# Performance work log

Measured on AMD Instinct MI355X. Metric: run time of the kernel, lower is better.

The kernel has to match this reference:

```python
import jax, jax.numpy as jnp
import numpy as np

N = 50000          # nodes
E = 800000         # edges (avg in-degree 16)
IN_FEATS = 256
H = 4              # num_heads
D = 32             # out_feats per head
NEG_SLOPE = 0.2


def setup_inputs() -> dict:
    key = jax.random.key(0)
    k1, k2, k3, k4, k5, k6 = jax.random.split(key, 6)
    feat = jax.random.normal(k1, (N, IN_FEATS), dtype=jnp.float32)
    src = jax.random.randint(k2, (E,), 0, N, dtype=jnp.int32)
    dst = jax.random.randint(k3, (E,), 0, N, dtype=jnp.int32)
    # parameters (xavier-ish scale)
    W = jax.random.normal(k4, (IN_FEATS, H * D), dtype=jnp.float32) * (2.0 / (IN_FEATS + H * D)) ** 0.5
    attn_l = jax.random.normal(k5, (H, D), dtype=jnp.float32) * 0.1
    attn_r = jax.random.normal(k6, (H, D), dtype=jnp.float32) * 0.1
    bias = jnp.zeros((H * D,), dtype=jnp.float32)
    return {"feat": feat, "src": src, "dst": dst, "W": W,
            "attn_l": attn_l, "attn_r": attn_r, "bias": bias}


def reference(feat, src, dst, W, attn_l, attn_r, bias):
    # dense projection: [N, H, D]
    ft = (feat @ W).reshape(N, H, D)
    # per-node attention logits: [N, H]
    el = jnp.einsum('nhd,hd->nh', ft, attn_l)
    er = jnp.einsum('nhd,hd->nh', ft, attn_r)
    # SDDMM u_add_v + leaky relu: per-edge scores [E, H]
    e = jax.nn.leaky_relu(el[src] + er[dst], negative_slope=NEG_SLOPE)
    # edge softmax over incoming edges of each dst node (segment softmax)
    m = jax.ops.segment_max(e, dst, num_segments=N)          # [N, H], -inf for empty
    e_exp = jnp.exp(e - m[dst])                               # [E, H]
    s = jax.ops.segment_sum(e_exp, dst, num_segments=N)       # [N, H]
    a = e_exp / s[dst]                                        # [E, H]
    # SpMM u_mul_e: weighted aggregation to dst nodes
    rst = jax.ops.segment_sum(ft[src] * a[:, :, None], dst, num_segments=N)  # [N, H, D]
    rst = rst + bias.reshape(1, H, D)
    return rst
```

## Files before the change

kernel.cpp:

```cpp
#include <hip/hip_runtime.h>
#include <hip/hip_bf16.h>
#include <math.h>

#define N_NODES 50000
#define N_EDGES 800000
#define IN_F 256
#define HD 128
#define NHEAD 4
#define NB_SCAN 196

typedef __attribute__((ext_vector_type(8))) short bf16x8;
typedef __attribute__((ext_vector_type(4))) float f32x4;

__device__ __forceinline__ float lrelu(float x){ return x > 0.f ? x : 0.2f * x; }

__device__ __forceinline__ unsigned short f32_to_bf16_rn(float x){
    union { float f; unsigned int u; } v; v.f = x;
    unsigned int r = v.u + 0x7FFFu + ((v.u >> 16) & 1u);
    return (unsigned short)(r >> 16);
}
__device__ __forceinline__ float bf16_to_f32(unsigned short h){
    union { unsigned int u; float f; } v; v.u = ((unsigned int)h) << 16;
    return v.f;
}
__device__ __forceinline__ float bflo(unsigned int u){
    union { unsigned int x; float f; } v; v.x = u << 16; return v.f;
}
__device__ __forceinline__ float bfhi(unsigned int u){
    union { unsigned int x; float f; } v; v.x = u & 0xFFFF0000u; return v.f;
}

__global__ void zero_ints(int* __restrict__ p, int n){
    int i = blockIdx.x * blockDim.x + threadIdx.x;
    if (i < n) p[i] = 0;
}

__global__ __launch_bounds__(256) void wsplit_kernel(const float* __restrict__ W,
                                                     unsigned short* __restrict__ Wt_hi,
                                                     unsigned short* __restrict__ Wt_lo){
    int gid = blockIdx.x * 256 + threadIdx.x;
    int n = gid >> 8;
    int k = gid & 255;
    float x = W[(size_t)k * HD + n];
    unsigned short h = f32_to_bf16_rn(x);
    float r = x - bf16_to_f32(h);
    unsigned short l = f32_to_bf16_rn(r);
    Wt_hi[gid] = h;
    Wt_lo[gid] = l;
}

__global__ __launch_bounds__(256) void gemm_kernel(const float* __restrict__ feat,
                                                   const unsigned short* __restrict__ Wt_hi,
                                                   const unsigned short* __restrict__ Wt_lo,
                                                   const float* __restrict__ attn_l,
                                                   const float* __restrict__ attn_r,
                                                   unsigned short* __restrict__ ftb,
                                                   float* __restrict__ el,
                                                   float* __restrict__ er){
    __shared__ unsigned short Ah[128][72];
    __shared__ unsigned short Al[128][72];
    __shared__ unsigned short Bh[128][72];
    __shared__ unsigned short Bl[128][72];

    const int tid  = threadIdx.x;
    const int lane = tid & 63;
    const int wave = tid >> 6;
    const int wrow = wave * 32;
    const int lrow = lane & 15;
    const int lkh  = (lane >> 4) * 8;
    const int row0 = blockIdx.x * 128;

    f32x4 acc[2][8];
#pragma unroll
    for (int i = 0; i < 2; i++)
#pragma unroll
        for (int j = 0; j < 8; j++) acc[i][j] = (f32x4){0.f, 0.f, 0.f, 0.f};

    const int srow = tid >> 1;
    const int skh  = (tid & 1) * 32;

    for (int kc = 0; kc < 4; ++kc){
        const int k0 = kc * 64;
        {
            int gr = row0 + srow;
            const float* fp = feat + (size_t)gr * IN_F + k0 + skh;
            unsigned short* ah = &Ah[srow][skh];
            unsigned short* al = &Al[srow][skh];
#pragma unroll
            for (int u = 0; u < 8; ++u){
                float4 v = make_float4(0.f,0.f,0.f,0.f);
                if (gr < N_NODES) v = *(const float4*)(fp + 4 * u);
                ushort4 h, l;
                h.x = f32_to_bf16_rn(v.x); l.x = f32_to_bf16_rn(v.x - bf16_to_f32(h.x));
                h.y = f32_to_bf16_rn(v.y); l.y = f32_to_bf16_rn(v.y - bf16_to_f32(h.y));
                h.z = f32_to_bf16_rn(v.z); l.z = f32_to_bf16_rn(v.z - bf16_to_f32(h.z));
                h.w = f32_to_bf16_rn(v.w); l.w = f32_to_bf16_rn(v.w - bf16_to_f32(h.w));
                *(ushort4*)(ah + 4 * u) = h;
                *(ushort4*)(al + 4 * u) = l;
            }
        }
        {
            const unsigned short* bh = Wt_hi + srow * 256 + k0 + skh;
            const unsigned short* bl = Wt_lo + srow * 256 + k0 + skh;
#pragma unroll
            for (int u = 0; u < 4; ++u){
                *(uint4*)(&Bh[srow][skh + 8 * u]) = *(const uint4*)(bh + 8 * u);
                *(uint4*)(&Bl[srow][skh + 8 * u]) = *(const uint4*)(bl + 8 * u);
            }
        }
        __syncthreads();
#pragma unroll
        for (int kk = 0; kk < 2; ++kk){
            const int kb = kk * 32 + lkh;
            bf16x8 ah0 = *(const bf16x8*)(&Ah[wrow + lrow][kb]);
            bf16x8 ah1 = *(const bf16x8*)(&Ah[wrow + 16 + lrow][kb]);
            bf16x8 al0 = *(const bf16x8*)(&Al[wrow + lrow][kb]);
            bf16x8 al1 = *(const bf16x8*)(&Al[wrow + 16 + lrow][kb]);
#pragma unroll
            for (int nf = 0; nf < 8; ++nf){
                bf16x8 bh = *(const bf16x8*)(&Bh[nf * 16 + lrow][kb]);
                bf16x8 bl = *(const bf16x8*)(&Bl[nf * 16 + lrow][kb]);
                acc[0][nf] = __builtin_amdgcn_mfma_f32_16x16x32_bf16(ah0, bh, acc[0][nf], 0, 0, 0);
                acc[1][nf] = __builtin_amdgcn_mfma_f32_16x16x32_bf16(ah1, bh, acc[1][nf], 0, 0, 0);
                acc[0][nf] = __builtin_amdgcn_mfma_f32_16x16x32_bf16(ah0, bl, acc[0][nf], 0, 0, 0);
                acc[1][nf] = __builtin_amdgcn_mfma_f32_16x16x32_bf16(ah1, bl, acc[1][nf], 0, 0, 0);
                acc[0][nf] = __builtin_amdgcn_mfma_f32_16x16x32_bf16(al0, bh, acc[0][nf], 0, 0, 0);
                acc[1][nf] = __builtin_amdgcn_mfma_f32_16x16x32_bf16(al1, bh, acc[1][nf], 0, 0, 0);
            }
        }
        __syncthreads();
    }
    float alv[8], arv[8];
#pragma unroll
    for (int nf = 0; nf < 8; ++nf){
        alv[nf] = attn_l[lrow + nf * 16];
        arv[nf] = attn_r[lrow + nf * 16];
    }
#pragma unroll
    for (int mf = 0; mf < 2; ++mf){
#pragma unroll
        for (int r = 0; r < 4; ++r){
            int gr = row0 + wrow + mf * 16 + (lane >> 4) * 4 + r;
            if (gr < N_NODES){
                unsigned short* op = ftb + (size_t)gr * HD + lrow;
#pragma unroll
                for (int nf = 0; nf < 8; ++nf) op[nf * 16] = f32_to_bf16_rn(acc[mf][nf][r]);
            }
            float pl0 = acc[mf][0][r] * alv[0] + acc[mf][1][r] * alv[1];
            float pl1 = acc[mf][2][r] * alv[2] + acc[mf][3][r] * alv[3];
            float pl2 = acc[mf][4][r] * alv[4] + acc[mf][5][r] * alv[5];
            float pl3 = acc[mf][6][r] * alv[6] + acc[mf][7][r] * alv[7];
            float pr0 = acc[mf][0][r] * arv[0] + acc[mf][1][r] * arv[1];
            float pr1 = acc[mf][2][r] * arv[2] + acc[mf][3][r] * arv[3];
            float pr2 = acc[mf][4][r] * arv[4] + acc[mf][5][r] * arv[5];
            float pr3 = acc[mf][6][r] * arv[6] + acc[mf][7][r] * arv[7];
#pragma unroll
            for (int m = 1; m <= 8; m <<= 1){
                pl0 += __shfl_xor(pl0, m, 64); pl1 += __shfl_xor(pl1, m, 64);
                pl2 += __shfl_xor(pl2, m, 64); pl3 += __shfl_xor(pl3, m, 64);
                pr0 += __shfl_xor(pr0, m, 64); pr1 += __shfl_xor(pr1, m, 64);
                pr2 += __shfl_xor(pr2, m, 64); pr3 += __shfl_xor(pr3, m, 64);
            }
            if ((lane & 15) == 0 && gr < N_NODES){
                *(float4*)(el + (size_t)gr * NHEAD) = make_float4(pl0, pl1, pl2, pl3);
                *(float4*)(er + (size_t)gr * NHEAD) = make_float4(pr0, pr1, pr2, pr3);
            }
        }
    }
}

__global__ void degree_kernel(const int* __restrict__ dst, int* __restrict__ deg,
                              int* __restrict__ rank){
    int e = blockIdx.x * blockDim.x + threadIdx.x;
    if (e < N_EDGES) rank[e] = atomicAdd(&deg[dst[e]], 1);
}

__global__ __launch_bounds__(256) void scan_part(const int* __restrict__ deg,
                                                 int* __restrict__ row_off,
                                                 int* __restrict__ blk_sums){
    __shared__ int lds[256];
    int tid = threadIdx.x;
    int i = blockIdx.x * 256 + tid;
    int v = (i < N_NODES) ? deg[i] : 0;
    int x = v;
    lds[tid] = x;
    __syncthreads();
    for (int off = 1; off < 256; off <<= 1){
        int t = (tid >= off) ? lds[tid - off] : 0;
        __syncthreads();
        x += t;
        lds[tid] = x;
        __syncthreads();
    }
    if (i < N_NODES) row_off[i] = x - v;
    if (tid == 255) blk_sums[blockIdx.x] = x;
}

__global__ __launch_bounds__(256) void scan_mid(int* __restrict__ blk_sums,
                                                int* __restrict__ blk_off){
    __shared__ int lds[256];
    int tid = threadIdx.x;
    int v = (tid < NB_SCAN) ? blk_sums[tid] : 0;
    int x = v;
    lds[tid] = x;
    __syncthreads();
    for (int off = 1; off < 256; off <<= 1){
        int t = (tid >= off) ? lds[tid - off] : 0;
        __syncthreads();
        x += t;
        lds[tid] = x;
        __syncthreads();
    }
    blk_off[tid] = x - v;
}

__global__ __launch_bounds__(256) void scan_add(int* __restrict__ row_off,
                                                const int* __restrict__ blk_off){
    int i = blockIdx.x * 256 + threadIdx.x;
    if (i < N_NODES) row_off[i] += blk_off[blockIdx.x];
    if (blockIdx.x == 0 && threadIdx.x == 0) row_off[N_NODES] = N_EDGES;
}

__global__ void scatter_kernel(const int* __restrict__ src, const int* __restrict__ dst,
                               const int* __restrict__ rank, const int* __restrict__ row_off,
                               int* __restrict__ csr_src){
    int e = blockIdx.x * blockDim.x + threadIdx.x;
    if (e >= N_EDGES) return;
    csr_src[row_off[dst[e]] + rank[e]] = src[e];
}

__global__ __launch_bounds__(256) void aggregate_kernel(const unsigned short* __restrict__ ftb,
                                                        const int* __restrict__ csr_src,
                                                        const float* __restrict__ el,
                                                        const float* __restrict__ er,
                                                        const int* __restrict__ row_off,
                                                        const float* __restrict__ bias,
                                                        float* __restrict__ out){
    __shared__ float lw[4][64][4];
    __shared__ int   ls[4][64];

    const int wv   = threadIdx.x >> 6;
    const int n    = blockIdx.x * 4 + wv;
    const int lane = threadIdx.x & 63;
    const int g    = lane >> 4;
    const int l    = lane & 15;
    const int h    = l >> 2;
    const int beg  = row_off[n], end = row_off[n + 1];
    const float4 ern = *(const float4*)(er + (size_t)n * NHEAD);

    float a[8];
#pragma unroll
    for (int k = 0; k < 8; ++k) a[k] = 0.f;
    float wsum = 0.f;

    for (int base = beg; base < end; base += 64){
        int cnt = end - base; if (cnt > 64) cnt = 64;
        float4 w4 = make_float4(0.f, 0.f, 0.f, 0.f);
        int s_l = 0;
        if (lane < cnt){
            s_l = csr_src[base + lane];
            float4 elv = *(const float4*)(el + (size_t)s_l * NHEAD);
            w4.x = __expf(lrelu(elv.x + ern.x));
            w4.y = __expf(lrelu(elv.y + ern.y));
            w4.z = __expf(lrelu(elv.z + ern.z));
            w4.w = __expf(lrelu(elv.w + ern.w));
        }
        ls[wv][lane] = s_l;
        *(float4*)(&lw[wv][lane][0]) = w4;
        asm volatile("s_waitcnt lgkmcnt(0)" ::: "memory");
        __builtin_amdgcn_sched_barrier(0);
        for (int j0 = 0; j0 < cnt; j0 += 4){
            int j = j0 + g;
            float w = lw[wv][j][h];
            int   s = ls[wv][j];
            uint4 f = *(const uint4*)(ftb + (size_t)s * HD + 8 * l);
            a[0] += w * bflo(f.x); a[1] += w * bfhi(f.x);
            a[2] += w * bflo(f.y); a[3] += w * bfhi(f.y);
            a[4] += w * bflo(f.z); a[5] += w * bfhi(f.z);
            a[6] += w * bflo(f.w); a[7] += w * bfhi(f.w);
            wsum += w;
        }
        __builtin_amdgcn_sched_barrier(0);
    }
#pragma unroll
    for (int m = 16; m <= 32; m <<= 1){
#pragma unroll
        for (int k = 0; k < 8; ++k) a[k] += __shfl_xor(a[k], m, 64);
        wsum += __shfl_xor(wsum, m, 64);
    }
    float inv = (end > beg) ? 1.f / wsum : 0.f;
    if (g < 2){
        int col = 8 * l + 4 * g;
        float4 b4 = *(const float4*)(bias + col);
        float4 o;
        o.x = a[4 * g + 0] * inv + b4.x;
        o.y = a[4 * g + 1] * inv + b4.y;
        o.z = a[4 * g + 2] * inv + b4.z;
        o.w = a[4 * g + 3] * inv + b4.w;
        *(float4*)(out + (size_t)n * HD + col) = o;
    }
}

extern "C" void kernel_launch(void* const* d_in, const int* in_sizes, int n_in,
                              void* d_out, int out_size, void* d_ws, size_t ws_size,
                              hipStream_t stream){
    const float* feat   = (const float*)d_in[0];
    const int*   src    = (const int*)  d_in[1];
    const int*   dst    = (const int*)  d_in[2];
    const float* W      = (const float*)d_in[3];
    const float* attn_l = (const float*)d_in[4];
    const float* attn_r = (const float*)d_in[5];
    const float* bias   = (const float*)d_in[6];
    float* out = (float*)d_out;
    char*  ws  = (char*)d_ws;

    unsigned short* ftb = (unsigned short*)(ws + 0);
    float* el      = (float*)(ws + 12800000);
    float* er      = (float*)(ws + 13600000);
    int*   deg     = (int*)  (ws + 14400000);
    int*   rank    = (int*)  (ws + 14600000);
    int*   row_off = (int*)  (ws + 17800000);
    int*   csr_src = (int*)  (ws + 18000064);

    unsigned short* Wt_hi = (unsigned short*)csr_src;
    unsigned short* Wt_lo = Wt_hi + 32768;
    int* blk_sums = (int*)(((char*)csr_src) + 131072);
    int* blk_off  = blk_sums + 256;

    zero_ints<<<(N_NODES + 255) / 256, 256, 0, stream>>>(deg, N_NODES);
    wsplit_kernel<<<128, 256, 0, stream>>>(W, Wt_hi, Wt_lo);
    gemm_kernel<<<(N_NODES + 127) / 128, 256, 0, stream>>>(feat, Wt_hi, Wt_lo,
                                                           attn_l, attn_r, ftb, el, er);
    degree_kernel<<<(N_EDGES + 255) / 256, 256, 0, stream>>>(dst, deg, rank);
    scan_part<<<NB_SCAN, 256, 0, stream>>>(deg, row_off, blk_sums);
    scan_mid<<<1, 256, 0, stream>>>(blk_sums, blk_off);
    scan_add<<<NB_SCAN, 256, 0, stream>>>(row_off, blk_off);
    scatter_kernel<<<(N_EDGES + 255) / 256, 256, 0, stream>>>(src, dst, rank, row_off, csr_src);
    aggregate_kernel<<<(N_NODES + 3) / 4, 256, 0, stream>>>(ftb, csr_src, el, er,
                                                            row_off, bias, out);
}
```

Baseline: 225.2 us.

## Load GEMM A fragments directly to registers and shrink row tile to 64

The projection GEMM now has each lane load its own fp32 feat fragment straight from global memory into registers and split it into bf16 hi/lo there, so the A tile no longer goes through LDS. B is stored in LDS pre-swizzled in MFMA fragment order. The row tile per block drops from 128 to 64, giving each wave one 16-row MFMA tile instead of two, and launch bounds ask for 4 blocks per CU. The aim is less LDS traffic and pressure, more occupancy and more blocks; the cost is that each block reloads W into LDS for half as many rows.

```diff
diff --git a/kernel.cpp b/kernel.cpp
--- a/kernel.cpp
+++ b/kernel.cpp
@@ -8,6 +8,7 @@
 #define HD 128
 #define NHEAD 4
 #define NB_SCAN 196
+#define GBM 64
 
 typedef __attribute__((ext_vector_type(8))) short bf16x8;
 typedef __attribute__((ext_vector_type(4))) float f32x4;
@@ -49,83 +50,67 @@
     Wt_lo[gid] = l;
 }
 
-__global__ __launch_bounds__(256) void gemm_kernel(const float* __restrict__ feat,
-                                                   const unsigned short* __restrict__ Wt_hi,
-                                                   const unsigned short* __restrict__ Wt_lo,
-                                                   const float* __restrict__ attn_l,
-                                                   const float* __restrict__ attn_r,
-                                                   unsigned short* __restrict__ ftb,
-                                                   float* __restrict__ el,
-                                                   float* __restrict__ er){
-    __shared__ unsigned short Ah[128][72];
-    __shared__ unsigned short Al[128][72];
-    __shared__ unsigned short Bh[128][72];
-    __shared__ unsigned short Bl[128][72];
+__global__ __launch_bounds__(256, 4) void gemm_kernel(const float* __restrict__ feat,
+                                                      const unsigned short* __restrict__ Wt_hi,
+                                                      const unsigned short* __restrict__ Wt_lo,
+                                                      const float* __restrict__ attn_l,
+                                                      const float* __restrict__ attn_r,
+                                                      unsigned short* __restrict__ ftb,
+                                                      float* __restrict__ el,
+                                                      float* __restrict__ er){
+    __shared__ unsigned short Bh[2][8][64][8];
+    __shared__ unsigned short Bl[2][8][64][8];
 
     const int tid  = threadIdx.x;
     const int lane = tid & 63;
-    const int wave = tid >> 6;
-    const int wrow = wave * 32;
-    const int lrow = lane & 15;
-    const int lkh  = (lane >> 4) * 8;
-    const int row0 = blockIdx.x * 128;
-
-    f32x4 acc[2][8];
-#pragma unroll
-    for (int i = 0; i < 2; i++)
-#pragma unroll
-        for (int j = 0; j < 8; j++) acc[i][j] = (f32x4){0.f, 0.f, 0.f, 0.f};
-
-    const int srow = tid >> 1;
-    const int skh  = (tid & 1) * 32;
+    const int wv   = tid >> 6;
+    const int r    = lane & 15;
+    const int g    = lane >> 4;
+    const int arow = blockIdx.x * GBM + wv * 16 + r;
+    const bool rowok = (arow < N_NODES);
+    const float* arp = feat + (size_t)arow * IN_F + g * 8;
+
+    f32x4 acc[8];
+#pragma unroll
+    for (int j = 0; j < 8; ++j) acc[j] = (f32x4){0.f, 0.f, 0.f, 0.f};
 
     for (int kc = 0; kc < 4; ++kc){
         const int k0 = kc * 64;
-        {
-            int gr = row0 + srow;
-            const float* fp = feat + (size_t)gr * IN_F + k0 + skh;
-            unsigned short* ah = &Ah[srow][skh];
-            unsigned short* al = &Al[srow][skh];
-#pragma unroll
-            for (int u = 0; u < 8; ++u){
-                float4 v = make_float4(0.f,0.f,0.f,0.f);
-                if (gr < N_NODES) v = *(const float4*)(fp + 4 * u);
-                ushort4 h, l;
-                h.x = f32_to_bf16_rn(v.x); l.x = f32_to_bf16_rn(v.x - bf16_to_f32(h.x));
-                h.y = f32_to_bf16_rn(v.y); l.y = f32_to_bf16_rn(v.y - bf16_to_f32(h.y));
-                h.z = f32_to_bf16_rn(v.z); l.z = f32_to_bf16_rn(v.z - bf16_to_f32(h.z));
-                h.w = f32_to_bf16_rn(v.w); l.w = f32_to_bf16_rn(v.w - bf16_to_f32(h.w));
-                *(ushort4*)(ah + 4 * u) = h;
-                *(ushort4*)(al + 4 * u) = l;
+#pragma unroll
+        for (int i = 0; i < 4; ++i){
+            int u  = tid * 4 + i;
+            int l2 = u & 63;
+            int fn = (u >> 6) & 7;
+            int kb = u >> 9;
+            int nn = fn * 16 + (l2 & 15);
+            int kk = k0 + kb * 32 + (l2 >> 4) * 8;
+            *(uint4*)(&Bh[kb][fn][l2][0]) = *(const uint4*)(Wt_hi + nn * 256 + kk);
+            *(uint4*)(&Bl[kb][fn][l2][0]) = *(const uint4*)(Wt_lo + nn * 256 + kk);
+        }
+        __syncthreads();
+#pragma unroll
+        for (int kb = 0; kb < 2; ++kb){
+            float4 v0 = make_float4(0.f, 0.f, 0.f, 0.f), v1 = v0;
+            if (rowok){
+                const float* fp = arp + k0 + kb * 32;
+                v0 = *(const float4*)(fp);
+                v1 = *(const float4*)(fp + 4);
             }
-        }
-        {
-            const unsigned short* bh = Wt_hi + srow * 256 + k0 + skh;
-            const unsigned short* bl = Wt_lo + srow * 256 + k0 + skh;
-#pragma unroll
-            for (int u = 0; u < 4; ++u){
-                *(uint4*)(&Bh[srow][skh + 8 * u]) = *(const uint4*)(bh + 8 * u);
-                *(uint4*)(&Bl[srow][skh + 8 * u]) = *(const uint4*)(bl + 8 * u);
+            float av[8] = {v0.x, v0.y, v0.z, v0.w, v1.x, v1.y, v1.z, v1.w};
+            bf16x8 ah, al;
+#pragma unroll
+            for (int j = 0; j < 8; ++j){
+                unsigned short h = f32_to_bf16_rn(av[j]);
+                ah[j] = (short)h;
+                al[j] = (short)f32_to_bf16_rn(av[j] - bf16_to_f32(h));
             }
-        }
-        __syncthreads();
-#pragma unroll
-        for (int kk = 0; kk < 2; ++kk){
-            const int kb = kk * 32 + lkh;
-            bf16x8 ah0 = *(const bf16x8*)(&Ah[wrow + lrow][kb]);
-            bf16x8 ah1 = *(const bf16x8*)(&Ah[wrow + 16 + lrow][kb]);
-            bf16x8 al0 = *(const bf16x8*)(&Al[wrow + lrow][kb]);
-            bf16x8 al1 = *(const bf16x8*)(&Al[wrow + 16 + lrow][kb]);
 #pragma unroll
             for (int nf = 0; nf < 8; ++nf){
-                bf16x8 bh = *(const bf16x8*)(&Bh[nf * 16 + lrow][kb]);
-                bf16x8 bl = *(const bf16x8*)(&Bl[nf * 16 + lrow][kb]);
-                acc[0][nf] = __builtin_amdgcn_mfma_f32_16x16x32_bf16(ah0, bh, acc[0][nf], 0, 0, 0);
-                acc[1][nf] = __builtin_amdgcn_mfma_f32_16x16x32_bf16(ah1, bh, acc[1][nf], 0, 0, 0);
-                acc[0][nf] = __builtin_amdgcn_mfma_f32_16x16x32_bf16(ah0, bl, acc[0][nf], 0, 0, 0);
-                acc[1][nf] = __builtin_amdgcn_mfma_f32_16x16x32_bf16(ah1, bl, acc[1][nf], 0, 0, 0);
-                acc[0][nf] = __builtin_amdgcn_mfma_f32_16x16x32_bf16(al0, bh, acc[0][nf], 0, 0, 0);
-                acc[1][nf] = __builtin_amdgcn_mfma_f32_16x16x32_bf16(al1, bh, acc[1][nf], 0, 0, 0);
+                bf16x8 bh = *(const bf16x8*)(&Bh[kb][nf][lane][0]);
+                bf16x8 bl = *(const bf16x8*)(&Bl[kb][nf][lane][0]);
+                acc[nf] = __builtin_amdgcn_mfma_f32_16x16x32_bf16(ah, bh, acc[nf], 0, 0, 0);
+                acc[nf] = __builtin_amdgcn_mfma_f32_16x16x32_bf16(ah, bl, acc[nf], 0, 0, 0);
+                acc[nf] = __builtin_amdgcn_mfma_f32_16x16x32_bf16(al, bh, acc[nf], 0, 0, 0);
             }
         }
         __syncthreads();
@@ -133,38 +118,36 @@
     float alv[8], arv[8];
 #pragma unroll
     for (int nf = 0; nf < 8; ++nf){
-        alv[nf] = attn_l[lrow + nf * 16];
-        arv[nf] = attn_r[lrow + nf * 16];
-    }
-#pragma unroll
-    for (int mf = 0; mf < 2; ++mf){
-#pragma unroll
-        for (int r = 0; r < 4; ++r){
-            int gr = row0 + wrow + mf * 16 + (lane >> 4) * 4 + r;
-            if (gr < N_NODES){
-                unsigned short* op = ftb + (size_t)gr * HD + lrow;
-#pragma unroll
-                for (int nf = 0; nf < 8; ++nf) op[nf * 16] = f32_to_bf16_rn(acc[mf][nf][r]);
-            }
-            float pl0 = acc[mf][0][r] * alv[0] + acc[mf][1][r] * alv[1];
-            float pl1 = acc[mf][2][r] * alv[2] + acc[mf][3][r] * alv[3];
-            float pl2 = acc[mf][4][r] * alv[4] + acc[mf][5][r] * alv[5];
-            float pl3 = acc[mf][6][r] * alv[6] + acc[mf][7][r] * alv[7];
-            float pr0 = acc[mf][0][r] * arv[0] + acc[mf][1][r] * arv[1];
-            float pr1 = acc[mf][2][r] * arv[2] + acc[mf][3][r] * arv[3];
-            float pr2 = acc[mf][4][r] * arv[4] + acc[mf][5][r] * arv[5];
-            float pr3 = acc[mf][6][r] * arv[6] + acc[mf][7][r] * arv[7];
-#pragma unroll
-            for (int m = 1; m <= 8; m <<= 1){
-                pl0 += __shfl_xor(pl0, m, 64); pl1 += __shfl_xor(pl1, m, 64);
-                pl2 += __shfl_xor(pl2, m, 64); pl3 += __shfl_xor(pl3, m, 64);
-                pr0 += __shfl_xor(pr0, m, 64); pr1 += __shfl_xor(pr1, m, 64);
-                pr2 += __shfl_xor(pr2, m, 64); pr3 += __shfl_xor(pr3, m, 64);
-            }
-            if ((lane & 15) == 0 && gr < N_NODES){
-                *(float4*)(el + (size_t)gr * NHEAD) = make_float4(pl0, pl1, pl2, pl3);
-                *(float4*)(er + (size_t)gr * NHEAD) = make_float4(pr0, pr1, pr2, pr3);
-            }
+        alv[nf] = attn_l[r + nf * 16];
+        arv[nf] = attn_r[r + nf * 16];
+    }
+    const int g4 = g * 4;
+#pragma unroll
+    for (int rg = 0; rg < 4; ++rg){
+        int gr = blockIdx.x * GBM + wv * 16 + g4 + rg;
+        if (gr < N_NODES){
+            unsigned short* op = ftb + (size_t)gr * HD + r;
+#pragma unroll
+            for (int nf = 0; nf < 8; ++nf) op[nf * 16] = f32_to_bf16_rn(acc[nf][rg]);
+        }
+        float pl0 = acc[0][rg] * alv[0] + acc[1][rg] * alv[1];
+        float pl1 = acc[2][rg] * alv[2] + acc[3][rg] * alv[3];
+        float pl2 = acc[4][rg] * alv[4] + acc[5][rg] * alv[5];
+        float pl3 = acc[6][rg] * alv[6] + acc[7][rg] * alv[7];
+        float pr0 = acc[0][rg] * arv[0] + acc[1][rg] * arv[1];
+        float pr1 = acc[2][rg] * arv[2] + acc[3][rg] * arv[3];
+        float pr2 = acc[4][rg] * arv[4] + acc[5][rg] * arv[5];
+        float pr3 = acc[6][rg] * arv[6] + acc[7][rg] * arv[7];
+#pragma unroll
+        for (int m = 1; m <= 8; m <<= 1){
+            pl0 += __shfl_xor(pl0, m, 64); pl1 += __shfl_xor(pl1, m, 64);
+            pl2 += __shfl_xor(pl2, m, 64); pl3 += __shfl_xor(pl3, m, 64);
+            pr0 += __shfl_xor(pr0, m, 64); pr1 += __shfl_xor(pr1, m, 64);
+            pr2 += __shfl_xor(pr2, m, 64); pr3 += __shfl_xor(pr3, m, 64);
+        }
+        if (r == 0 && gr < N_NODES){
+            *(float4*)(el + (size_t)gr * NHEAD) = make_float4(pl0, pl1, pl2, pl3);
+            *(float4*)(er + (size_t)gr * NHEAD) = make_float4(pr0, pr1, pr2, pr3);
         }
     }
 }
@@ -329,8 +312,8 @@
 
     zero_ints<<<(N_NODES + 255) / 256, 256, 0, stream>>>(deg, N_NODES);
     wsplit_kernel<<<128, 256, 0, stream>>>(W, Wt_hi, Wt_lo);
-    gemm_kernel<<<(N_NODES + 127) / 128, 256, 0, stream>>>(feat, Wt_hi, Wt_lo,
-                                                           attn_l, attn_r, ftb, el, er);
+    gemm_kernel<<<(N_NODES + GBM - 1) / GBM, 256, 0, stream>>>(feat, Wt_hi, Wt_lo,
+                                                               attn_l, attn_r, ftb, el, er);
     degree_kernel<<<(N_EDGES + 255) / 256, 256, 0, stream>>>(dst, deg, rank);
     scan_part<<<NB_SCAN, 256, 0, stream>>>(deg, row_off, blk_sums);
     scan_mid<<<1, 256, 0, stream>>>(blk_sums, blk_off);
```

Result: no change. 222.8 us (-1.1%).
